# Optimization experiments

Hardware: AMD Instinct MI355X
Metric: run time of the kernel (lower is better)

The kernel has to match this reference:

```python
import jax, jax.numpy as jnp
import numpy as np

NC = 80          # num classes
REG_MAX = 16     # DFL bins
STRIDES = (8, 16, 32)
FEAT_HW = ((80, 80), (40, 40), (20, 20))
MAX_DET = 100
CONF_THRES = 0.25
IOU_THRES = 0.45
PRE_TOPK = 1000  # pre-NMS candidate count (EfficientNMS-style preselection)


def setup_inputs() -> dict:
    key = jax.random.key(0)
    k1, k2, k3 = jax.random.split(key, 3)
    B = 32
    no = 4 * REG_MAX + NC  # 144
    return {
        "p3": jax.random.normal(k1, (B, no, 80, 80), dtype=jnp.float32),
        "p4": jax.random.normal(k2, (B, no, 40, 40), dtype=jnp.float32),
        "p5": jax.random.normal(k3, (B, no, 20, 20), dtype=jnp.float32),
    }


def _make_anchors():
    # grid_cell_offset = 0.5, matching ultralytics make_anchors
    pts, strs = [], []
    for (h, w), s in zip(FEAT_HW, STRIDES):
        sx = jnp.arange(w, dtype=jnp.float32) + 0.5
        sy = jnp.arange(h, dtype=jnp.float32) + 0.5
        yy, xx = jnp.meshgrid(sy, sx, indexing="ij")
        pts.append(jnp.stack([xx.ravel(), yy.ravel()], axis=-1))  # [h*w, 2]
        strs.append(jnp.full((h * w, 1), float(s), dtype=jnp.float32))
    return jnp.concatenate(pts, 0), jnp.concatenate(strs, 0)  # [A,2], [A,1]


def _pairwise_iou(b):
    # b: [K, 4] xyxy
    area = (b[:, 2] - b[:, 0]) * (b[:, 3] - b[:, 1])
    lt = jnp.maximum(b[:, None, :2], b[None, :, :2])
    rb = jnp.minimum(b[:, None, 2:], b[None, :, 2:])
    wh = jnp.clip(rb - lt, 0.0)
    inter = wh[..., 0] * wh[..., 1]
    return inter / (area[:, None] + area[None, :] - inter + 1e-7)


def _nms_single(bxyxy, conf):
    # Greedy class-agnostic NMS over PRE_TOPK score-sorted boxes.
    K = bxyxy.shape[0]
    iou = _pairwise_iou(bxyxy)  # [K, K]
    idx = jnp.arange(K)

    def step(suppressed, xs):
        i, row = xs
        keep = jnp.logical_and(jnp.logical_not(suppressed[i]), conf[i] > 0.0)
        suppressed = jnp.logical_or(suppressed, keep & (row > IOU_THRES) & (idx > i))
        return suppressed, keep

    _, keeps = jax.lax.scan(step, jnp.zeros(K, dtype=bool), (idx, iou))
    return keeps  # [K] bool


def reference(p3, p4, p5):
    feats = [p3, p4, p5]
    B = p3.shape[0]
    no = 4 * REG_MAX + NC
    # concat across scales: [B, no, A]
    x_cat = jnp.concatenate([f.reshape(B, no, -1) for f in feats], axis=2)
    box, cls = x_cat[:, : 4 * REG_MAX], x_cat[:, 4 * REG_MAX:]

    anchors, strd = _make_anchors()  # [A,2], [A,1]
    A = box.shape[-1]

    # DFL: softmax over reg_max bins, expectation with arange weights
    prob = jax.nn.softmax(box.reshape(B, 4, REG_MAX, A), axis=2)
    dist = jnp.einsum("bkra,r->bka", prob, jnp.arange(REG_MAX, dtype=jnp.float32))

    # dist2bbox (xywh) then scale by stride
    anc = anchors.T  # [2, A]
    lt, rb = dist[:, :2], dist[:, 2:]
    x1y1 = anc - lt
    x2y2 = anc + rb
    dbox = jnp.concatenate([(x1y1 + x2y2) * 0.5, x2y2 - x1y1], axis=1) * strd.T  # [B,4,A]

    boxes = dbox.transpose(0, 2, 1)                       # [B, A, 4] xywh
    scores = jax.nn.sigmoid(cls).transpose(0, 2, 1)       # [B, A, NC] (score_activation=1)

    # class-agnostic: best class per box
    conf = scores.max(-1)                                 # [B, A]
    cls_id = jnp.argmax(scores, -1)                       # [B, A]
    conf_m = jnp.where(conf > CONF_THRES, conf, -1.0)

    topv, topi = jax.lax.top_k(conf_m, PRE_TOPK)          # [B, K]
    bsel = jnp.take_along_axis(boxes, topi[..., None], axis=1)  # [B, K, 4]
    cx, cy, w, h = bsel[..., 0], bsel[..., 1], bsel[..., 2], bsel[..., 3]
    bxyxy = jnp.stack([cx - w * 0.5, cy - h * 0.5, cx + w * 0.5, cy + h * 0.5], -1)

    keeps = jax.vmap(_nms_single)(bxyxy, topv)            # [B, K]
    kept_scores = jnp.where(keeps, topv, -1.0)
    dv, di = jax.lax.top_k(kept_scores, MAX_DET)          # [B, MAX_DET]
    valid = dv > 0.0

    det_scores = jnp.where(valid, dv, 0.0)
    det_boxes = jnp.take_along_axis(bxyxy, di[..., None], axis=1) * valid[..., None]
    sel_cls = jnp.take_along_axis(jnp.take_along_axis(cls_id, topi, 1), di, 1)
    det_classes = jnp.where(valid, sel_cls, 0).astype(jnp.int32)
    num_dets = valid.sum(-1, keepdims=True).astype(jnp.int32)
    return num_dets, det_boxes, det_scores, det_classes
```

## Files before the change

kernel.cpp:

```cpp
#include <hip/hip_runtime.h>
#include <math.h>

#define NCLS 80
#define NA 8400
#define NB 32
#define NO 144
#define PRE_TOPK 1000
#define MAX_DET 100

template<int HW, int WDIM, int S>
__device__ __forceinline__ void decode_blk(
    const float* __restrict__ src, int b, int a0, int aoff,
    float* __restrict__ conf, int* __restrict__ clsid, float* __restrict__ box)
{
    __shared__ float s_dfl[64 * 5];
    __shared__ float s_mx[64 * 5];
    __shared__ int   s_id[64 * 5];

    int t  = threadIdx.x;
    int p  = t >> 6;
    int al = t & 63;
    int pos = a0 + al;
    int posc = pos < HW ? pos : HW - 1;
    const float* base = src + (size_t)b * (NO * HW) + posc;

    float v[16], c[20];
    #pragma unroll
    for (int r = 0; r < 16; ++r) v[r] = base[(size_t)(p * 16 + r) * HW];
    #pragma unroll
    for (int cc = 0; cc < 20; ++cc) c[cc] = base[(size_t)(64 + p * 20 + cc) * HW];

    float mm = v[0];
    #pragma unroll
    for (int r = 1; r < 16; ++r) mm = fmaxf(mm, v[r]);
    float sum = 0.f, d = 0.f;
    #pragma unroll
    for (int r = 0; r < 16; ++r) {
        float e = __expf(v[r] - mm);
        sum += e;
        d += e * (float)r;
    }
    d *= 1.0f / sum;

    float m = c[0]; int ii = 0;
    #pragma unroll
    for (int cc = 1; cc < 20; ++cc) if (c[cc] > m) { m = c[cc]; ii = cc; }

    s_dfl[al * 5 + p] = d;
    s_mx[al * 5 + p]  = m;
    s_id[al * 5 + p]  = p * 20 + ii;
    __syncthreads();

    if (t < 64 && a0 + t < HW) {
        int pos2 = a0 + t;
        float d0 = s_dfl[t * 5 + 0], d1 = s_dfl[t * 5 + 1];
        float d2 = s_dfl[t * 5 + 2], d3 = s_dfl[t * 5 + 3];
        float bm = s_mx[t * 5 + 0]; int bid = s_id[t * 5 + 0];
        float m1 = s_mx[t * 5 + 1]; if (m1 > bm) { bm = m1; bid = s_id[t * 5 + 1]; }
        float m2 = s_mx[t * 5 + 2]; if (m2 > bm) { bm = m2; bid = s_id[t * 5 + 2]; }
        float m3 = s_mx[t * 5 + 3]; if (m3 > bm) { bm = m3; bid = s_id[t * 5 + 3]; }
        float conf_v = 1.0f / (1.0f + __expf(-bm));

        float ax = (float)(pos2 % WDIM) + 0.5f;
        float ay = (float)(pos2 / WDIM) + 0.5f;
        float x1 = ax - d0, y1 = ay - d1;
        float x2 = ax + d2, y2 = ay + d3;
        float cx = ((x1 + x2) * 0.5f) * (float)S;
        float cy = ((y1 + y2) * 0.5f) * (float)S;
        float w  = (x2 - x1) * (float)S;
        float h  = (y2 - y1) * (float)S;

        size_t gid = (size_t)b * NA + aoff + pos2;
        conf[gid]  = conf_v;
        clsid[gid] = bid;
        *(float4*)(box + gid * 4) = make_float4(cx, cy, w, h);
    }
}

__global__ __launch_bounds__(256) void k_decode(
    const float* __restrict__ p3, const float* __restrict__ p4, const float* __restrict__ p5,
    float* __restrict__ conf, int* __restrict__ clsid, float* __restrict__ box)
{
    int blk = blockIdx.x;
    int b = blk / 132;
    int r = blk - b * 132;
    if (r < 100)       decode_blk<6400, 80, 8>(p3, b, r * 64, 0, conf, clsid, box);
    else if (r < 125)  decode_blk<1600, 40, 16>(p4, b, (r - 100) * 64, 6400, conf, clsid, box);
    else               decode_blk<400, 20, 32>(p5, b, (r - 125) * 64, 8000, conf, clsid, box);
}

__device__ __forceinline__ uint32_t ord_bits(float f) {
    uint32_t u = __float_as_uint(f);
    return (u & 0x80000000u) ? ~u : (u | 0x80000000u);
}

__global__ __launch_bounds__(1024) void k_select(
    const float* __restrict__ conf, const float* __restrict__ box, const int* __restrict__ clsid,
    float* __restrict__ topv, float* __restrict__ bxyxy, int* __restrict__ topcls)
{
    int b = blockIdx.x;
    int t = threadIdx.x;
    int lane = t & 63;

    __shared__ uint32_t ob[NA];
    __shared__ uint32_t hist[256];
    __shared__ uint64_t sbuf[1024];
    __shared__ uint64_t s_prefix;
    __shared__ int s_k;
    __shared__ int s_cnt;

    const float* cf = conf + (size_t)b * NA;
    for (int i = t; i < NA; i += 1024) {
        float c = cf[i];
        float cm = (c > 0.25f) ? c : -1.0f;
        ob[i] = ord_bits(cm);
    }
    if (t == 0) { s_prefix = 0; s_k = PRE_TOPK; s_cnt = 0; }
    sbuf[t] = 0;
    __syncthreads();

    for (int pass = 0; pass < 8; ++pass) {
        int shift = 56 - 8 * pass;
        if (t < 256) hist[t] = 0;
        __syncthreads();
        uint64_t prefix = s_prefix;
        int k = s_k;
        for (int i = t; i < NA; i += 1024) {
            uint64_t key = ((uint64_t)ob[i] << 32) | (uint64_t)(0xFFFFFFFFu - (uint32_t)i);
            bool match = (pass == 0) || (((key ^ prefix) >> (64 - 8 * pass)) == 0);
            uint32_t d = (uint32_t)(key >> shift) & 255u;
            if (match) {
                uint64_t m = __ballot(1);
                #pragma unroll
                for (int bb = 0; bb < 8; ++bb) {
                    uint64_t bal = __ballot((d >> bb) & 1u);
                    m &= ((d >> bb) & 1u) ? bal : ~bal;
                }
                if ((m & ((1ull << lane) - 1ull)) == 0ull)
                    atomicAdd(&hist[d], (uint32_t)__popcll(m));
            }
        }
        __syncthreads();
        if (t < 64) {
            uint32_t h0 = hist[4 * t + 0], h1 = hist[4 * t + 1];
            uint32_t h2 = hist[4 * t + 2], h3 = hist[4 * t + 3];
            uint32_t part = h0 + h1 + h2 + h3;
            uint32_t s = part;
            #pragma unroll
            for (int off = 1; off < 64; off <<= 1) {
                uint32_t v = __shfl_down(s, off);
                if (t + off < 64) s += v;
            }
            uint32_t cb3 = s - part;
            uint32_t cb2 = cb3 + h3;
            uint32_t cb1 = cb2 + h2;
            uint32_t cb0 = cb1 + h1;
            uint32_t ku = (uint32_t)k;
            if (cb3 < ku && ku <= cb3 + h3) { s_k = k - (int)cb3; s_prefix = prefix | ((uint64_t)(uint32_t)(4 * t + 3) << shift); }
            if (cb2 < ku && ku <= cb2 + h2) { s_k = k - (int)cb2; s_prefix = prefix | ((uint64_t)(uint32_t)(4 * t + 2) << shift); }
            if (cb1 < ku && ku <= cb1 + h1) { s_k = k - (int)cb1; s_prefix = prefix | ((uint64_t)(uint32_t)(4 * t + 1) << shift); }
            if (cb0 < ku && ku <= cb0 + h0) { s_k = k - (int)cb0; s_prefix = prefix | ((uint64_t)(uint32_t)(4 * t + 0) << shift); }
        }
        __syncthreads();
    }

    uint64_t kstar = s_prefix;
    for (int i = t; i < NA; i += 1024) {
        uint64_t key = ((uint64_t)ob[i] << 32) | (uint64_t)(0xFFFFFFFFu - (uint32_t)i);
        if (key >= kstar) {
            int p = atomicAdd(&s_cnt, 1);
            if (p < 1024) sbuf[p] = key;
        }
    }
    __syncthreads();

    uint64_t v = sbuf[t];
    for (int k = 2; k <= 1024; k <<= 1) {
        for (int j = k >> 1; j > 0; j >>= 1) {
            uint64_t o;
            if (j >= 64) {
                sbuf[t] = v;
                __syncthreads();
                o = sbuf[t ^ j];
                __syncthreads();
            } else {
                o = __shfl_xor((unsigned long long)v, j);
            }
            bool desc  = ((t & k) == 0);
            bool lower = ((t & j) == 0);
            v = (desc == lower) ? (v > o ? v : o) : (v < o ? v : o);
        }
    }

    if (t < PRE_TOPK) {
        uint64_t key = v;
        uint32_t u = (uint32_t)(key >> 32);
        uint32_t fb = (u & 0x80000000u) ? (u ^ 0x80000000u) : ~u;
        float val = __uint_as_float(fb);
        int idx = (int)(0xFFFFFFFFu - (uint32_t)(key & 0xFFFFFFFFull));
        size_t g = (size_t)b * NA + idx;
        float4 bx = *(const float4*)(box + g * 4);
        float cx = bx.x, cy = bx.y, w = bx.z, h = bx.w;
        size_t o = (size_t)b * PRE_TOPK + t;
        topv[o] = val;
        *(float4*)(bxyxy + o * 4) = make_float4(cx - w * 0.5f, cy - h * 0.5f,
                                                cx + w * 0.5f, cy + h * 0.5f);
        topcls[o] = clsid[g];
    }
}

__device__ __forceinline__ int bslot(int j) { return j + (j >> 6); }

__global__ __launch_bounds__(256) void k_iou(
    const float* __restrict__ bxyxy, unsigned long long* __restrict__ mask)
{
    __shared__ float4 boxes[PRE_TOPK + 16];
    int b = blockIdx.y;
    int t = threadIdx.x;
    const float4* bp = (const float4*)(bxyxy + (size_t)b * PRE_TOPK * 4);
    for (int i = t; i < PRE_TOPK; i += 256) boxes[bslot(i)] = bp[i];
    __syncthreads();

    int r_local = t >> 4, w = t & 15;
    int row = blockIdx.x * 16 + r_local;
    if (row >= PRE_TOPK) return;

    float4 bi = boxes[bslot(row)];
    float area_i = (bi.z - bi.x) * (bi.w - bi.y);
    unsigned long long bits = 0;
    int j0 = w * 64;
    #pragma unroll 4
    for (int jj = 0; jj < 64; ++jj) {
        int j = j0 + jj;
        if (j >= PRE_TOPK) break;
        if (j <= row) continue;
        float4 bj = boxes[bslot(j)];
        float lx = fmaxf(bi.x, bj.x), ly = fmaxf(bi.y, bj.y);
        float rx = fminf(bi.z, bj.z), ry = fminf(bi.w, bj.w);
        float iw = fmaxf(rx - lx, 0.f), ih = fmaxf(ry - ly, 0.f);
        float inter = iw * ih;
        float area_j = (bj.z - bj.x) * (bj.w - bj.y);
        float iou = inter / (area_i + area_j - inter + 1e-7f);
        if (iou > 0.45f) bits |= (1ull << jj);
    }
    mask[((size_t)b * PRE_TOPK + row) * 16 + w] = bits;
}

__global__ __launch_bounds__(1024) void k_nms(
    const unsigned long long* __restrict__ mask, const float* __restrict__ topv,
    const float* __restrict__ bxyxy, const int* __restrict__ topcls,
    float* __restrict__ out)
{
    int b = blockIdx.x;
    int t = threadIdx.x;

    __shared__ __align__(16) unsigned long long smask[PRE_TOPK * 16];
    __shared__ float sv[PRE_TOPK];
    __shared__ unsigned long long s_valid[16];
    __shared__ int kept[MAX_DET];
    __shared__ int s_cnt;

    for (int i = t; i < PRE_TOPK; i += 1024) sv[i] = topv[(size_t)b * PRE_TOPK + i];
    {
        const ulonglong2* src = (const ulonglong2*)(mask + (size_t)b * PRE_TOPK * 16);
        ulonglong2* dst = (ulonglong2*)smask;
        for (int i = t; i < PRE_TOPK * 8; i += 1024) dst[i] = src[i];
    }
    __syncthreads();

    {
        bool pred = (t < PRE_TOPK) && (sv[t] > 0.0f);
        unsigned long long bal = __ballot(pred);
        if ((t & 63) == 0) s_valid[t >> 6] = bal;
    }
    __syncthreads();

    if (t < 64) {
        int w = t;
        unsigned long long supp = 0;
        unsigned long long valid = (w < 16) ? s_valid[w] : 0ull;
        int base = w * 64;
        int cur = -1;
        int cnt = 0;
        while (cnt < MAX_DET) {
            unsigned long long gt;
            if (cur < base)            gt = ~0ull;
            else if (cur - base >= 63) gt = 0ull;
            else                       gt = (~0ull) << (cur - base + 1);
            unsigned long long cand = valid & ~supp & gt;
            int idx = cand ? (base + __builtin_ctzll(cand)) : 0x7FFFFFFF;
            #pragma unroll
            for (int off = 8; off >= 1; off >>= 1) {
                int o = __shfl_xor(idx, off);
                idx = (o < idx) ? o : idx;
            }
            int nxt = __shfl(idx, 0);
            if (nxt == 0x7FFFFFFF) break;
            if (t == 0) kept[cnt] = nxt;
            ++cnt;
            if (w < 16) supp |= smask[nxt * 16 + w];
            cur = nxt;
        }
        if (t == 0) s_cnt = cnt;
    }
    __syncthreads();

    int cnt = s_cnt; if (cnt > MAX_DET) cnt = MAX_DET;
    if (t == 0) out[b] = (float)cnt;
    if (t < MAX_DET) {
        bool valid = t < cnt;
        float bx0 = 0.f, bx1 = 0.f, bx2 = 0.f, bx3 = 0.f, sc = 0.f, cl = 0.f;
        if (valid) {
            int p = kept[t];
            size_t o = (size_t)b * PRE_TOPK + p;
            float4 bb = *(const float4*)(bxyxy + o * 4);
            bx0 = bb.x; bx1 = bb.y; bx2 = bb.z; bx3 = bb.w;
            sc = sv[p];
            cl = (float)topcls[o];
        }
        size_t db = 32 + ((size_t)b * MAX_DET + t) * 4;
        out[db + 0] = bx0; out[db + 1] = bx1; out[db + 2] = bx2; out[db + 3] = bx3;
        out[32 + 12800 + (size_t)b * MAX_DET + t] = sc;
        out[32 + 16000 + (size_t)b * MAX_DET + t] = cl;
    }
}

extern "C" void kernel_launch(void* const* d_in, const int* in_sizes, int n_in,
                              void* d_out, int out_size, void* d_ws, size_t ws_size,
                              hipStream_t stream)
{
    const float* p3 = (const float*)d_in[0];
    const float* p4 = (const float*)d_in[1];
    const float* p5 = (const float*)d_in[2];
    float* out = (float*)d_out;

    char* ws = (char*)d_ws;
    size_t off_mask = 0;
    size_t off_conf = off_mask + (size_t)NB * PRE_TOPK * 16 * 8;
    size_t off_cls  = off_conf + (size_t)NB * NA * 4;
    size_t off_box  = off_cls  + (size_t)NB * NA * 4;
    size_t off_topv = off_box  + (size_t)NB * NA * 4 * 4;
    size_t off_topc = off_topv + (size_t)NB * PRE_TOPK * 4;
    size_t off_bx   = off_topc + (size_t)NB * PRE_TOPK * 4;

    unsigned long long* mask = (unsigned long long*)(ws + off_mask);
    float* conf   = (float*)(ws + off_conf);
    int*   clsid  = (int*)(ws + off_cls);
    float* box    = (float*)(ws + off_box);
    float* topv   = (float*)(ws + off_topv);
    int*   topcls = (int*)(ws + off_topc);
    float* bxyxy  = (float*)(ws + off_bx);

    k_decode<<<NB * 132, 256, 0, stream>>>(p3, p4, p5, conf, clsid, box);
    k_select<<<NB, 1024, 0, stream>>>(conf, box, clsid, topv, bxyxy, topcls);
    k_iou<<<dim3((PRE_TOPK + 15) / 16, NB), 256, 0, stream>>>(bxyxy, mask);
    k_nms<<<NB, 1024, 0, stream>>>(mask, topv, bxyxy, topcls, out);
}
```

Measured before the change: 142.1 us.

## Stage decode tile via float4 loads into shared memory; shrink radix-select key to 46 bits

The decode kernel now loads the whole 144-channel by 64-anchor tile with vectorized float4 global loads into shared memory, then reads per-thread channel values from LDS instead of issuing scalar strided global loads. The shared tile is reused for the reduction scratch. Separately, the top-k radix select packs score bits and a 14-bit index into a 46-bit key, cutting the histogram passes from 8 to 6. This adds a larger LDS footprint per block, which could limit occupancy, and an extra barrier.

```diff
diff --git a/kernel.cpp b/kernel.cpp
--- a/kernel.cpp
+++ b/kernel.cpp
@@ -11,25 +11,32 @@
 template<int HW, int WDIM, int S>
 __device__ __forceinline__ void decode_blk(
     const float* __restrict__ src, int b, int a0, int aoff,
-    float* __restrict__ conf, int* __restrict__ clsid, float* __restrict__ box)
-{
-    __shared__ float s_dfl[64 * 5];
-    __shared__ float s_mx[64 * 5];
-    __shared__ int   s_id[64 * 5];
-
-    int t  = threadIdx.x;
-    int p  = t >> 6;
-    int al = t & 63;
-    int pos = a0 + al;
-    int posc = pos < HW ? pos : HW - 1;
-    const float* base = src + (size_t)b * (NO * HW) + posc;
-
-    float v[16], c[20];
-    #pragma unroll
-    for (int r = 0; r < 16; ++r) v[r] = base[(size_t)(p * 16 + r) * HW];
-    #pragma unroll
-    for (int cc = 0; cc < 20; ++cc) c[cc] = base[(size_t)(64 + p * 20 + cc) * HW];
-
+    float* __restrict__ conf, int* __restrict__ clsid, float* __restrict__ box,
+    float* s_tile)
+{
+    int t = threadIdx.x;
+    int w = t >> 6;
+    int l = t & 63;
+
+    {
+        int ch_base = w * 36;
+        int chl = ch_base + (l >> 4);
+        int aq = (l & 15) * 4;
+        int aqc = a0 + aq; if (aqc > HW - 4) aqc = HW - 4;
+        const float* gsrc = src + ((size_t)b * NO) * HW + aqc;
+        float4 stg[9];
+        #pragma unroll
+        for (int i = 0; i < 9; ++i)
+            stg[i] = *(const float4*)(gsrc + (size_t)(chl + i * 4) * HW);
+        #pragma unroll
+        for (int i = 0; i < 9; ++i)
+            *(float4*)&s_tile[(chl + i * 4) * 64 + aq] = stg[i];
+    }
+    __syncthreads();
+
+    float v[16];
+    #pragma unroll
+    for (int r = 0; r < 16; ++r) v[r] = s_tile[(w * 16 + r) * 64 + l];
     float mm = v[0];
     #pragma unroll
     for (int r = 1; r < 16; ++r) mm = fmaxf(mm, v[r]);
@@ -42,13 +49,21 @@
     }
     d *= 1.0f / sum;
 
+    float c[20];
+    #pragma unroll
+    for (int cc = 0; cc < 20; ++cc) c[cc] = s_tile[(64 + w * 20 + cc) * 64 + l];
     float m = c[0]; int ii = 0;
     #pragma unroll
     for (int cc = 1; cc < 20; ++cc) if (c[cc] > m) { m = c[cc]; ii = cc; }
 
-    s_dfl[al * 5 + p] = d;
-    s_mx[al * 5 + p]  = m;
-    s_id[al * 5 + p]  = p * 20 + ii;
+    __syncthreads();
+
+    float* s_dfl = s_tile;
+    float* s_mx  = s_tile + 320;
+    int*   s_id  = (int*)(s_tile + 640);
+    s_dfl[l * 5 + w] = d;
+    s_mx[l * 5 + w]  = m;
+    s_id[l * 5 + w]  = w * 20 + ii;
     __syncthreads();
 
     if (t < 64 && a0 + t < HW) {
@@ -67,13 +82,13 @@
         float x2 = ax + d2, y2 = ay + d3;
         float cx = ((x1 + x2) * 0.5f) * (float)S;
         float cy = ((y1 + y2) * 0.5f) * (float)S;
-        float w  = (x2 - x1) * (float)S;
-        float h  = (y2 - y1) * (float)S;
+        float ww = (x2 - x1) * (float)S;
+        float hh = (y2 - y1) * (float)S;
 
         size_t gid = (size_t)b * NA + aoff + pos2;
         conf[gid]  = conf_v;
         clsid[gid] = bid;
-        *(float4*)(box + gid * 4) = make_float4(cx, cy, w, h);
+        *(float4*)(box + gid * 4) = make_float4(cx, cy, ww, hh);
     }
 }
 
@@ -81,12 +96,13 @@
     const float* __restrict__ p3, const float* __restrict__ p4, const float* __restrict__ p5,
     float* __restrict__ conf, int* __restrict__ clsid, float* __restrict__ box)
 {
+    __shared__ float s_tile[NO * 64];
     int blk = blockIdx.x;
     int b = blk / 132;
     int r = blk - b * 132;
-    if (r < 100)       decode_blk<6400, 80, 8>(p3, b, r * 64, 0, conf, clsid, box);
-    else if (r < 125)  decode_blk<1600, 40, 16>(p4, b, (r - 100) * 64, 6400, conf, clsid, box);
-    else               decode_blk<400, 20, 32>(p5, b, (r - 125) * 64, 8000, conf, clsid, box);
+    if (r < 100)       decode_blk<6400, 80, 8>(p3, b, r * 64, 0, conf, clsid, box, s_tile);
+    else if (r < 125)  decode_blk<1600, 40, 16>(p4, b, (r - 100) * 64, 6400, conf, clsid, box, s_tile);
+    else               decode_blk<400, 20, 32>(p5, b, (r - 125) * 64, 8000, conf, clsid, box, s_tile);
 }
 
 __device__ __forceinline__ uint32_t ord_bits(float f) {
@@ -119,15 +135,15 @@
     sbuf[t] = 0;
     __syncthreads();
 
-    for (int pass = 0; pass < 8; ++pass) {
-        int shift = 56 - 8 * pass;
+    for (int pass = 0; pass < 6; ++pass) {
+        int shift = 40 - 8 * pass;
         if (t < 256) hist[t] = 0;
         __syncthreads();
         uint64_t prefix = s_prefix;
         int k = s_k;
         for (int i = t; i < NA; i += 1024) {
-            uint64_t key = ((uint64_t)ob[i] << 32) | (uint64_t)(0xFFFFFFFFu - (uint32_t)i);
-            bool match = (pass == 0) || (((key ^ prefix) >> (64 - 8 * pass)) == 0);
+            uint64_t key = ((uint64_t)ob[i] << 14) | (uint64_t)(16383 - i);
+            bool match = (pass == 0) || (((key ^ prefix) >> (48 - 8 * pass)) == 0);
             uint32_t d = (uint32_t)(key >> shift) & 255u;
             if (match) {
                 uint64_t m = __ballot(1);
@@ -166,7 +182,7 @@
 
     uint64_t kstar = s_prefix;
     for (int i = t; i < NA; i += 1024) {
-        uint64_t key = ((uint64_t)ob[i] << 32) | (uint64_t)(0xFFFFFFFFu - (uint32_t)i);
+        uint64_t key = ((uint64_t)ob[i] << 14) | (uint64_t)(16383 - i);
         if (key >= kstar) {
             int p = atomicAdd(&s_cnt, 1);
             if (p < 1024) sbuf[p] = key;
@@ -194,10 +210,10 @@
 
     if (t < PRE_TOPK) {
         uint64_t key = v;
-        uint32_t u = (uint32_t)(key >> 32);
+        uint32_t u = (uint32_t)(key >> 14);
         uint32_t fb = (u & 0x80000000u) ? (u ^ 0x80000000u) : ~u;
         float val = __uint_as_float(fb);
-        int idx = (int)(0xFFFFFFFFu - (uint32_t)(key & 0xFFFFFFFFull));
+        int idx = 16383 - (int)(key & 16383u);
         size_t g = (size_t)b * NA + idx;
         float4 bx = *(const float4*)(box + g * 4);
         float cx = bx.x, cy = bx.y, w = bx.z, h = bx.w;
```

Measured after the change: 140.5 us. Within noise of the previous version (-1.1%).
